# Kernel optimization log

Measured on AMD Instinct MI355X. Metric: run time of the kernel, lower is better.

Reference implementation:

```python
import jax, jax.numpy as jnp
import numpy as np
from jax import lax

BN_EPS = 1e-5


def conv3x3(x, w):
    # x: [B,C,H,W], w: [O,I,3,3] -> [B,O,H,W], stride 1, SAME padding, no bias
    return lax.conv_general_dilated(x, w, (1, 1), 'SAME',
                                    dimension_numbers=('NCHW', 'OIHW', 'NCHW'))


def batchnorm_eval(x, gamma, beta, mean, var):
    inv = gamma / jnp.sqrt(var + BN_EPS)
    return x * inv[None, :, None, None] + (beta - mean * inv)[None, :, None, None]


def avg_pool3(x):
    # AvgPool2d(3, stride=1, padding=1) with count_include_pad=True -> sum/9
    s = lax.reduce_window(x, 0.0, lax.add, (1, 1, 3, 3), (1, 1, 1, 1), 'SAME')
    return s / 9.0


def max_pool3(x):
    return lax.reduce_window(x, -jnp.inf, lax.max, (1, 1, 3, 3), (1, 1, 1, 1), 'SAME')


def setup_inputs() -> dict:
    key = jax.random.key(0)
    ks = jax.random.split(key, 20)
    B, C, H, W = 8, 256, 48, 48
    sc = 0.05
    inp = {
        'ftr': jax.random.normal(ks[0], (B, C, H, W), jnp.float32),
        'wq': jax.random.normal(ks[1], (C, C, 1, 1), jnp.float32) * sc,
        'bq': jax.random.normal(ks[2], (C,), jnp.float32) * sc,
        'wk': jax.random.normal(ks[3], (C, C, 1, 1), jnp.float32) * sc,
        'bk': jax.random.normal(ks[4], (C,), jnp.float32) * sc,
        'wv': jax.random.normal(ks[5], (C, C, 1, 1), jnp.float32) * sc,
        'bv': jax.random.normal(ks[6], (C,), jnp.float32) * sc,
        'delta': jnp.array([0.1], jnp.float32),
        'w_rbc': jax.random.normal(ks[7], (C, C, 3, 3), jnp.float32) * sc,
        'g1': jnp.ones((C,), jnp.float32),
        'b1': jnp.zeros((C,), jnp.float32),
        'm1': jnp.zeros((C,), jnp.float32),
        'v1': jnp.ones((C,), jnp.float32),
        'w_rbc2': jax.random.normal(ks[8], (C, 2 * C, 3, 3), jnp.float32) * sc,
        'g2': jnp.ones((C,), jnp.float32),
        'b2': jnp.zeros((C,), jnp.float32),
        'm2': jnp.zeros((C,), jnp.float32),
        'v2': jnp.ones((C,), jnp.float32),
    }
    return inp


def reference(ftr, wq, bq, wk, bk, wv, bv, delta, w_rbc, g1, b1, m1, v1,
              w_rbc2, g2, b2, m2, v2):
    B, C, H, W = ftr.shape
    P = H * W
    x = ftr.reshape(B, C, P)  # [B,C,P]
    # 1x1 convs as channel matmuls
    q = jnp.einsum('oc,bcp->bop', wq[:, :, 0, 0], x) + bq[None, :, None]
    k = jnp.einsum('oc,bcp->bop', wk[:, :, 0, 0], x) + bk[None, :, None]
    v = jnp.einsum('oc,bcp->bop', wv[:, :, 0, 0], x) + bv[None, :, None]
    # scores[b,i,j] = sum_c q[b,c,i] * k[b,c,j]; softmax over i (dim=1)
    scores = jnp.einsum('bci,bcj->bij', q, k)
    weights = jax.nn.softmax(scores, axis=1)
    G = jnp.einsum('bci,bij->bcj', v, weights).reshape(B, C, H, W)
    out = delta[0] * G + ftr
    # conv_rbc: conv3x3 -> BN(eval) -> ReLU, then sigmoid gate
    out = jax.nn.relu(batchnorm_eval(conv3x3(out, w_rbc), g1, b1, m1, v1))
    gate = jax.nn.sigmoid(out)
    ftr_avg = avg_pool3(ftr) * gate
    ftr_max = max_pool3(ftr) * gate
    cat = jnp.concatenate((ftr_max, ftr_avg), axis=1)  # [B,2C,H,W]
    out = jax.nn.relu(batchnorm_eval(conv3x3(cat, w_rbc2), g2, b2, m2, v2))
    return out
```

## Files before the change

### kernel.cpp

```cpp
#include <hip/hip_runtime.h>
#include <math.h>

#define NB   8
#define CCH  256
#define PPX  2304
#define CPb  (CCH*PPX)
#define NTOT (NB*CPb)
#define PSQ  (PPX*PPX)
#define PADIMG 2500

typedef short short8_t __attribute__((ext_vector_type(8)));
typedef float f4_t __attribute__((ext_vector_type(4)));

__device__ __forceinline__ float relu_(float x){ return x > 0.f ? x : 0.f; }

__device__ __forceinline__ unsigned short f2bf(float f) {
  unsigned int u = __builtin_bit_cast(unsigned int, f);
  u += 0x7fffu + ((u >> 16) & 1u);
  return (unsigned short)(u >> 16);
}
__device__ __forceinline__ float bf2f(unsigned short h) {
  unsigned int u = ((unsigned int)h) << 16;
  return __builtin_bit_cast(float, u);
}
__device__ __forceinline__ unsigned int pack2(float a, float b) {
  return (unsigned int)f2bf(a) | ((unsigned int)f2bf(b) << 16);
}

__device__ __forceinline__ void gll16(const void* g, void* l) {
  __builtin_amdgcn_global_load_lds(
      (const __attribute__((address_space(1))) unsigned int*)g,
      (__attribute__((address_space(3))) unsigned int*)l, 16, 0, 0);
}

__global__ __launch_bounds__(256) void castw(
    const float* __restrict__ w, unsigned short* __restrict__ o, int n)
{
  const int i = blockIdx.x * 256 + threadIdx.x;
  if (i < n) o[i] = f2bf(w[i]);
}

__global__ __launch_bounds__(256) void repack_w(
    const float* __restrict__ w, unsigned short* __restrict__ wr, int Cin)
{
  const int idx = blockIdx.x * 256 + threadIdx.x;
  const int total = 9 * 256 * Cin;
  if (idx >= total) return;
  const int c = idx % Cin;
  const int rest = idx / Cin;
  const int o = rest % 256;
  const int tap = rest / 256;
  wr[idx] = f2bf(w[((size_t)o * Cin + c) * 9 + tap]);
}

__global__ __launch_bounds__(256) void transpose_cast(
    const float* __restrict__ ftr, unsigned short* __restrict__ xt)
{
  const int p0 = blockIdx.x * 64, c0 = blockIdx.y * 64, b = blockIdx.z;
  const int t = threadIdx.x;
  __shared__ unsigned short T[64][72];
  #pragma unroll
  for (int pass = 0; pass < 4; pass++) {
    const int cr = pass * 16 + (t >> 4);
    const int pc = (t & 15) * 4;
    float4 v = *(const float4*)&ftr[((size_t)(b * 256 + c0 + cr)) * PPX + p0 + pc];
    T[pc + 0][cr] = f2bf(v.x); T[pc + 1][cr] = f2bf(v.y);
    T[pc + 2][cr] = f2bf(v.z); T[pc + 3][cr] = f2bf(v.w);
  }
  __syncthreads();
  #pragma unroll
  for (int pass = 0; pass < 2; pass++) {
    const int pr = pass * 32 + (t >> 3);
    const int cc = (t & 7) * 8;
    *(uint4*)&xt[((size_t)(b * PPX + p0 + pr)) * 256 + c0 + cc] = *(const uint4*)&T[pr][cc];
  }
}

template<int EPI>
__global__ __launch_bounds__(256) void gemm_nt(
    const unsigned short* __restrict__ A, long Ab,
    const unsigned short* __restrict__ B, long Bb, int K,
    unsigned short* __restrict__ O, long Ob, int ldo,
    const float* __restrict__ bias,
    const float* __restrict__ ftr, const float* __restrict__ delta, int bstart)
{
  const int t = threadIdx.x;
  const int ln = t & 63;
  const int wid = t >> 6;
  const int wm = (wid & 1) * 64, wn = (wid >> 1) * 64;
  const int lm = ln & 15, lg = ln >> 4;
  const int m0 = blockIdx.x * 128, n0 = blockIdx.y * 128;
  const long bz = blockIdx.z;
  const unsigned short* Ap = A + bz * Ab;
  const unsigned short* Bp = B + bz * Bb;

  __shared__ __align__(16) unsigned short As[128 * 32];
  __shared__ __align__(16) unsigned short Bs[128 * 32];

  const int sR = ln >> 2, sP = ln & 3;
  const int fbase = lm * 32 + (((lg + (lm >> 2)) & 3) * 8);

  f4_t acc[4][4];
  #pragma unroll
  for (int i = 0; i < 4; i++)
    #pragma unroll
    for (int j = 0; j < 4; j++) acc[i][j] = (f4_t){0.f, 0.f, 0.f, 0.f};

  for (int k0 = 0; k0 < K; k0 += 32) {
    __syncthreads();
    #pragma unroll
    for (int i = wid; i < 8; i += 4) {
      const int R = i * 16 + sR;
      const int l = (sP - (R >> 2)) & 3;
      gll16(Ap + (size_t)(m0 + R) * K + k0 + l * 8, As + i * 512);
      gll16(Bp + (size_t)(n0 + R) * K + k0 + l * 8, Bs + i * 512);
    }
    __syncthreads();
    short8_t a[4], b[4];
    #pragma unroll
    for (int ti = 0; ti < 4; ti++)
      a[ti] = *(const short8_t*)(As + (wm + ti * 16) * 32 + fbase);
    #pragma unroll
    for (int tj = 0; tj < 4; tj++)
      b[tj] = *(const short8_t*)(Bs + (wn + tj * 16) * 32 + fbase);
    #pragma unroll
    for (int ti = 0; ti < 4; ti++)
      #pragma unroll
      for (int tj = 0; tj < 4; tj++)
        acc[ti][tj] = __builtin_amdgcn_mfma_f32_16x16x32_bf16(
            a[ti], b[tj], acc[ti][tj], 0, 0, 0);
  }

  if (EPI == 3) {
    const int b = bstart + (int)bz;
    const float d0 = delta[0];
    #pragma unroll
    for (int ti = 0; ti < 4; ti++) {
      const int mb = m0 + wm + ti * 16 + (lg << 2);
      #pragma unroll
      for (int tj = 0; tj < 4; tj++) {
        const int n = n0 + wn + tj * 16 + lm;
        const int y = n / 48, x = n - (n / 48) * 48;
        const size_t pp = (size_t)(y + 1) * 50 + (x + 1);
        float vr[4];
        #pragma unroll
        for (int r = 0; r < 4; r++)
          vr[r] = d0 * acc[ti][tj][r] + ftr[((size_t)(b * 256 + mb + r)) * PPX + n];
        uint2 o;
        o.x = pack2(vr[0], vr[1]);
        o.y = pack2(vr[2], vr[3]);
        *(uint2*)(O + ((size_t)b * PADIMG + pp) * 256 + mb) = o;
      }
    }
  } else {
    #pragma unroll
    for (int ti = 0; ti < 4; ti++) {
      const int mb = m0 + wm + ti * 16 + (lg << 2);
      #pragma unroll
      for (int tj = 0; tj < 4; tj++) {
        const int n = n0 + wn + tj * 16 + lm;
        float add0 = 0.f, add1 = 0.f, add2 = 0.f, add3 = 0.f;
        if (EPI == 1) { add0 = bias[mb]; add1 = bias[mb+1]; add2 = bias[mb+2]; add3 = bias[mb+3]; }
        if (EPI == 2) { add0 = add1 = add2 = add3 = bias[n]; }
        uint2 o;
        o.x = pack2(acc[ti][tj][0] + add0, acc[ti][tj][1] + add1);
        o.y = pack2(acc[ti][tj][2] + add2, acc[ti][tj][3] + add3);
        *(uint2*)(O + bz * Ob + (size_t)n * ldo + mb) = o;
      }
    }
  }
}

__global__ __launch_bounds__(256) void rowstats(
    unsigned short* __restrict__ St, long sstride)
{
  const int j = blockIdx.x, bb = blockIdx.y;
  unsigned short* row = St + (long)bb * sstride + (size_t)j * PPX;
  const int t = threadIdx.x;

  float v[16];
  int nv = 0;
  float m = -1e30f;
  for (int ch = t; ch < 288; ch += 256) {
    const uint4 d = *(const uint4*)(row + ch * 8);
    const unsigned int* dp = (const unsigned int*)&d;
    #pragma unroll
    for (int q = 0; q < 4; q++) {
      v[nv]     = bf2f((unsigned short)(dp[q] & 0xffffu));
      v[nv + 1] = bf2f((unsigned short)(dp[q] >> 16));
      m = fmaxf(m, fmaxf(v[nv], v[nv + 1]));
      nv += 2;
    }
  }
  #pragma unroll
  for (int off = 32; off > 0; off >>= 1)
    m = fmaxf(m, __shfl_xor(m, off));
  __shared__ float red[8];
  if ((t & 63) == 0) red[t >> 6] = m;
  __syncthreads();
  m = fmaxf(fmaxf(red[0], red[1]), fmaxf(red[2], red[3]));

  float sum = 0.f;
  for (int u = 0; u < nv; u++) { v[u] = __expf(v[u] - m); sum += v[u]; }
  #pragma unroll
  for (int off = 32; off > 0; off >>= 1)
    sum += __shfl_xor(sum, off);
  if ((t & 63) == 0) red[4 + (t >> 6)] = sum;
  __syncthreads();
  const float inv = 1.f / (red[4] + red[5] + red[6] + red[7]);

  int u = 0;
  for (int ch = t; ch < 288; ch += 256) {
    unsigned int res[4];
    #pragma unroll
    for (int q = 0; q < 4; q++) {
      res[q] = pack2(v[u] * inv, v[u + 1] * inv);
      u += 2;
    }
    *(uint4*)(row + ch * 8) = *(const uint4*)res;
  }
}

template<bool OUT_BF16>
__global__ __launch_bounds__(128) void conv_mfma(
    const unsigned short* __restrict__ act_p, int Cin,
    const unsigned short* __restrict__ wr,
    const float* __restrict__ gamma, const float* __restrict__ beta,
    const float* __restrict__ mean,  const float* __restrict__ var,
    void* __restrict__ outv)
{
  const int t  = threadIdx.x;
  const int wv = t >> 6;
  const int ln = t & 63;
  const int lm = ln & 15;
  const int lg = ln >> 4;

  const int bx = blockIdx.x;
  const int bb = bx / 18;
  const int p0 = (bx % 18) * 128;
  const int m0 = blockIdx.y * 64;

  __shared__ __align__(16) unsigned short Bs[240 * 32];
  __shared__ __align__(16) unsigned short As[9 * 64 * 32];

  const int qbase = p0 + 2 * (p0 / 48);
  int qoff[4];
  #pragma unroll
  for (int tj = 0; tj < 4; tj++) {
    const int p = p0 + wv * 64 + tj * 16 + lm;
    qoff[tj] = (p - p0) + 2 * (p / 48 - p0 / 48) + 51;
  }

  const int sR = ln >> 2, sP = ln & 3;
  const int abase = lm * 32 + (((lg + (lm >> 2)) & 3) * 8);

  f4_t acc[4][4];
  #pragma unroll
  for (int i = 0; i < 4; i++)
    #pragma unroll
    for (int j = 0; j < 4; j++) acc[i][j] = (f4_t){0.f, 0.f, 0.f, 0.f};

  for (int c0 = 0; c0 < Cin; c0 += 32) {
    __syncthreads();
    const unsigned short* gb = act_p + ((size_t)bb * PADIMG) * Cin + c0;
    for (int i = wv; i < 15; i += 2) {
      const int R = i * 16 + sR;
      int Rg = qbase + R;
      if (Rg > PADIMG - 1) Rg = PADIMG - 1;
      const int l = (sP - (R >> 2)) & 3;
      gll16(gb + (size_t)Rg * Cin + l * 8, Bs + i * 512);
    }
    for (int i = wv; i < 36; i += 2) {
      const int R = i * 16 + sR;
      const int tap = R >> 6, mr = R & 63;
      const int l = (sP - (R >> 2)) & 3;
      gll16(wr + ((size_t)(tap * 256 + m0 + mr)) * Cin + c0 + l * 8, As + i * 512);
    }
    __syncthreads();
    #pragma unroll
    for (int ky = 0; ky < 3; ky++) {
      #pragma unroll
      for (int kx = 0; kx < 3; kx++) {
        const int off = (ky - 1) * 50 + (kx - 1);
        const int tap = ky * 3 + kx;
        short8_t a[4], b[4];
        #pragma unroll
        for (int ti = 0; ti < 4; ti++)
          a[ti] = *(const short8_t*)(As + tap * 2048 + ti * 512 + abase);
        #pragma unroll
        for (int tj = 0; tj < 4; tj++) {
          const int R = qoff[tj] + off;
          const int slot = (lg + (R >> 2)) & 3;
          b[tj] = *(const short8_t*)(Bs + R * 32 + slot * 8);
        }
        #pragma unroll
        for (int ti = 0; ti < 4; ti++)
          #pragma unroll
          for (int tj = 0; tj < 4; tj++)
            acc[ti][tj] = __builtin_amdgcn_mfma_f32_16x16x32_bf16(
                a[ti], b[tj], acc[ti][tj], 0, 0, 0);
      }
    }
  }

  #pragma unroll
  for (int ti = 0; ti < 4; ti++) {
    const int m = m0 + ti * 16 + (lg << 2);
    float inv[4], add[4];
    #pragma unroll
    for (int r = 0; r < 4; r++) {
      inv[r] = gamma[m + r] * rsqrtf(var[m + r] + 1e-5f);
      add[r] = beta[m + r] - mean[m + r] * inv[r];
    }
    #pragma unroll
    for (int tj = 0; tj < 4; tj++) {
      const int p = p0 + wv * 64 + tj * 16 + lm;
      float vr[4];
      #pragma unroll
      for (int r = 0; r < 4; r++)
        vr[r] = relu_(acc[ti][tj][r] * inv[r] + add[r]);
      if (OUT_BF16) {
        uint2 o;
        o.x = pack2(vr[0], vr[1]);
        o.y = pack2(vr[2], vr[3]);
        *(uint2*)((unsigned short*)outv + ((size_t)(bb * PPX + p)) * 256 + m) = o;
      } else {
        #pragma unroll
        for (int r = 0; r < 4; r++)
          ((float*)outv)[((size_t)(bb * 256 + m + r)) * PPX + p] = vr[r];
      }
    }
  }
}

__global__ __launch_bounds__(256) void pool_gate_cat(
    const unsigned short* __restrict__ xt, const unsigned short* __restrict__ act1b,
    unsigned short* __restrict__ cat_p)
{
  const int idx = blockIdx.x * 256 + threadIdx.x;
  const int c = idx & 255;
  const int rest = idx >> 8;
  const int p = rest % PPX;
  const int b = rest / PPX;
  const int y = p / 48, x = p - (p / 48) * 48;
  const unsigned short* base = xt + ((size_t)b * PPX) * 256 + c;
  float s = 0.f, mxv = -1e30f;
  #pragma unroll
  for (int dy = -1; dy <= 1; dy++) {
    const int yy = y + dy;
    if (yy < 0 || yy >= 48) continue;
    #pragma unroll
    for (int dx = -1; dx <= 1; dx++) {
      const int xx = x + dx;
      if (xx < 0 || xx >= 48) continue;
      const float f = bf2f(base[(size_t)(yy * 48 + xx) * 256]);
      s += f; mxv = fmaxf(mxv, f);
    }
  }
  const float g = bf2f(act1b[(size_t)idx]);
  const float gate = 1.f / (1.f + __expf(-g));
  const size_t pp = (size_t)(y + 1) * 50 + (x + 1);
  unsigned short* crow = cat_p + ((size_t)b * PADIMG + pp) * 512;
  crow[c]       = f2bf(mxv * gate);
  crow[c + 256] = f2bf(s * (1.f / 9.f) * gate);
}

extern "C" void kernel_launch(void* const* d_in, const int* in_sizes, int n_in,
                              void* d_out, int out_size, void* d_ws, size_t ws_size,
                              hipStream_t stream)
{
  const float* ftr  = (const float*)d_in[0];
  const float* wq   = (const float*)d_in[1];
  const float* bq   = (const float*)d_in[2];
  const float* wk   = (const float*)d_in[3];
  const float* bk   = (const float*)d_in[4];
  const float* wv   = (const float*)d_in[5];
  const float* bv   = (const float*)d_in[6];
  const float* delta= (const float*)d_in[7];
  const float* w1   = (const float*)d_in[8];
  const float* g1   = (const float*)d_in[9];
  const float* b1   = (const float*)d_in[10];
  const float* m1   = (const float*)d_in[11];
  const float* v1   = (const float*)d_in[12];
  const float* w2   = (const float*)d_in[13];
  const float* g2   = (const float*)d_in[14];
  const float* b2   = (const float*)d_in[15];
  const float* m2   = (const float*)d_in[16];
  const float* v2   = (const float*)d_in[17];
  float* out = (float*)d_out;

  const size_t XT = (size_t)NTOT;
  unsigned short* base = (unsigned short*)d_ws;
  unsigned short* xt   = base;
  unsigned short* qt   = xt  + XT;
  unsigned short* kt   = qt  + XT;
  unsigned short* vbuf = kt  + XT;
  unsigned short* wqb  = vbuf + XT;
  unsigned short* wkb  = wqb + 65536;
  unsigned short* wvb  = wkb + 65536;
  unsigned short* wr1  = wvb + 65536;
  unsigned short* wr2  = wr1 + (size_t)9 * 256 * 256;
  unsigned short* attn_p = wr2 + (size_t)9 * 256 * 512;
  unsigned short* act1b  = attn_p + (size_t)NB * PADIMG * 256;
  unsigned short* cat_p  = act1b + XT;
  unsigned short* St     = cat_p + (size_t)NB * PADIMG * 512;

  const size_t head_bytes = (size_t)((char*)St - (char*)base);
  const bool modeA = ws_size >= head_bytes + (size_t)NB * PSQ * 2;

  const size_t ATTN_P_SH = (size_t)NB * PADIMG * 256;
  const size_t CAT_P_SH  = (size_t)NB * PADIMG * 512;

  castw<<<dim3(256), 256, 0, stream>>>(wq, wqb, 65536);
  castw<<<dim3(256), 256, 0, stream>>>(wk, wkb, 65536);
  castw<<<dim3(256), 256, 0, stream>>>(wv, wvb, 65536);
  repack_w<<<dim3((9 * 256 * 256 + 255) / 256), 256, 0, stream>>>(w1, wr1, 256);
  repack_w<<<dim3((9 * 256 * 512 + 255) / 256), 256, 0, stream>>>(w2, wr2, 512);

  transpose_cast<<<dim3(36, 4, 8), 256, 0, stream>>>(ftr, xt);

  gemm_nt<1><<<dim3(2, 18, 8), 256, 0, stream>>>(
      wqb, 0L, xt, (long)CPb, 256, qt, (long)CPb, 256, bq, nullptr, nullptr, 0);
  gemm_nt<1><<<dim3(2, 18, 8), 256, 0, stream>>>(
      wkb, 0L, xt, (long)CPb, 256, kt, (long)CPb, 256, bk, nullptr, nullptr, 0);
  gemm_nt<2><<<dim3(18, 2, 8), 256, 0, stream>>>(
      xt, (long)CPb, wvb, 0L, 256, vbuf, (long)CPb, PPX, bv, nullptr, nullptr, 0);

  hipMemsetAsync(attn_p, 0, ATTN_P_SH * 2, stream);

  if (modeA) {
    gemm_nt<0><<<dim3(18, 18, 8), 256, 0, stream>>>(
        qt, (long)CPb, kt, (long)CPb, 256, St, (long)PSQ, PPX, nullptr, nullptr, nullptr, 0);
    rowstats<<<dim3(PPX, 8), 256, 0, stream>>>(St, (long)PSQ);
    gemm_nt<3><<<dim3(2, 18, 8), 256, 0, stream>>>(
        vbuf, (long)CPb, St, (long)PSQ, PPX, attn_p, 0L, 0, nullptr, ftr, delta, 0);
  } else {
    for (int b = 0; b < NB; b++) {
      gemm_nt<0><<<dim3(18, 18, 1), 256, 0, stream>>>(
          qt + (size_t)b * CPb, 0L, kt + (size_t)b * CPb, 0L, 256,
          St, 0L, PPX, nullptr, nullptr, nullptr, 0);
      rowstats<<<dim3(PPX, 1), 256, 0, stream>>>(St, 0L);
      gemm_nt<3><<<dim3(2, 18, 1), 256, 0, stream>>>(
          vbuf + (size_t)b * CPb, 0L, St, 0L, PPX, attn_p, 0L, 0, nullptr, ftr, delta, b);
    }
  }

  conv_mfma<true><<<dim3(144, 4), 128, 0, stream>>>(
      attn_p, 256, wr1, g1, b1, m1, v1, (void*)act1b);

  hipMemsetAsync(cat_p, 0, CAT_P_SH * 2, stream);
  pool_gate_cat<<<dim3(NTOT / 256), 256, 0, stream>>>(xt, act1b, cat_p);

  conv_mfma<false><<<dim3(144, 4), 128, 0, stream>>>(
      cat_p, 512, wr2, g2, b2, m2, v2, (void*)out);
}
```

Baseline: 444.0 us.

## Double-buffer conv activation tiles and load weights directly into registers

Restructures the 3x3 conv MFMA kernel to use 256-thread blocks covering 256 pixels by 32 output channels. Weights no longer go through shared memory; each lane loads its A fragments straight from global memory into registers. The activation tile is double-buffered, so the next channel slice's global-to-LDS copy overlaps the current slice's MFMAs, and there is one barrier per iteration instead of two. The cost is heavier register pressure from holding 18 A fragments per lane, plus uncoalesced, redundant global weight reads across blocks.

```diff
diff --git a/kernel.cpp b/kernel.cpp
--- a/kernel.cpp
+++ b/kernel.cpp
@@ -222,7 +222,7 @@
 }
 
 template<bool OUT_BF16>
-__global__ __launch_bounds__(128) void conv_mfma(
+__global__ __launch_bounds__(256, 2) void conv_mfma(
     const unsigned short* __restrict__ act_p, int Cin,
     const unsigned short* __restrict__ wr,
     const float* __restrict__ gamma, const float* __restrict__ beta,
@@ -236,12 +236,11 @@
   const int lg = ln >> 4;
 
   const int bx = blockIdx.x;
-  const int bb = bx / 18;
-  const int p0 = (bx % 18) * 128;
-  const int m0 = blockIdx.y * 64;
-
-  __shared__ __align__(16) unsigned short Bs[240 * 32];
-  __shared__ __align__(16) unsigned short As[9 * 64 * 32];
+  const int bb = bx / 9;
+  const int p0 = (bx % 9) * 256;
+  const int m0 = blockIdx.y * 32;
+
+  __shared__ __align__(16) unsigned short Bs[2][368 * 32];
 
   const int qbase = p0 + 2 * (p0 / 48);
   int qoff[4];
@@ -252,59 +251,65 @@
   }
 
   const int sR = ln >> 2, sP = ln & 3;
-  const int abase = lm * 32 + (((lg + (lm >> 2)) & 3) * 8);
-
-  f4_t acc[4][4];
-  #pragma unroll
-  for (int i = 0; i < 4; i++)
+  const int sl = (sP - (sR >> 2)) & 3;
+
+  const unsigned short* wbase = wr + (size_t)(m0 + lm) * Cin + lg * 8;
+  const unsigned short* gb = act_p + (size_t)bb * PADIMG * Cin;
+  const unsigned short* gsrc = gb + (size_t)(qbase + sR) * Cin + sl * 8;
+
+  f4_t acc[2][4];
+  #pragma unroll
+  for (int i = 0; i < 2; i++)
     #pragma unroll
     for (int j = 0; j < 4; j++) acc[i][j] = (f4_t){0.f, 0.f, 0.f, 0.f};
 
-  for (int c0 = 0; c0 < Cin; c0 += 32) {
-    __syncthreads();
-    const unsigned short* gb = act_p + ((size_t)bb * PADIMG) * Cin + c0;
-    for (int i = wv; i < 15; i += 2) {
-      const int R = i * 16 + sR;
-      int Rg = qbase + R;
-      if (Rg > PADIMG - 1) Rg = PADIMG - 1;
-      const int l = (sP - (R >> 2)) & 3;
-      gll16(gb + (size_t)Rg * Cin + l * 8, Bs + i * 512);
-    }
-    for (int i = wv; i < 36; i += 2) {
-      const int R = i * 16 + sR;
-      const int tap = R >> 6, mr = R & 63;
-      const int l = (sP - (R >> 2)) & 3;
-      gll16(wr + ((size_t)(tap * 256 + m0 + mr)) * Cin + c0 + l * 8, As + i * 512);
-    }
-    __syncthreads();
+  const int nsl = Cin >> 5;
+
+  for (int i = wv; i < 23; i += 4)
+    gll16(gsrc + (size_t)i * 16 * Cin, &Bs[0][i * 512]);
+  __syncthreads();
+
+  int buf = 0;
+  for (int s = 0; s < nsl; s++) {
+    const int c0 = s * 32;
+    short8_t a[9][2];
+    #pragma unroll
+    for (int tap = 0; tap < 9; tap++)
+      #pragma unroll
+      for (int ti = 0; ti < 2; ti++)
+        a[tap][ti] = *(const short8_t*)(wbase + ((size_t)(tap * 256 + ti * 16)) * Cin + c0);
+    if (s + 1 < nsl) {
+      const unsigned short* src = gsrc + (c0 + 32);
+      for (int i = wv; i < 23; i += 4)
+        gll16(src + (size_t)i * 16 * Cin, &Bs[buf ^ 1][i * 512]);
+    }
     #pragma unroll
     for (int ky = 0; ky < 3; ky++) {
       #pragma unroll
       for (int kx = 0; kx < 3; kx++) {
         const int off = (ky - 1) * 50 + (kx - 1);
         const int tap = ky * 3 + kx;
-        short8_t a[4], b[4];
-        #pragma unroll
-        for (int ti = 0; ti < 4; ti++)
-          a[ti] = *(const short8_t*)(As + tap * 2048 + ti * 512 + abase);
+        short8_t b[4];
         #pragma unroll
         for (int tj = 0; tj < 4; tj++) {
           const int R = qoff[tj] + off;
           const int slot = (lg + (R >> 2)) & 3;
-          b[tj] = *(const short8_t*)(Bs + R * 32 + slot * 8);
+          b[tj] = *(const short8_t*)(&Bs[buf][R * 32 + slot * 8]);
         }
         #pragma unroll
-        for (int ti = 0; ti < 4; ti++)
+        for (int ti = 0; ti < 2; ti++)
           #pragma unroll
           for (int tj = 0; tj < 4; tj++)
             acc[ti][tj] = __builtin_amdgcn_mfma_f32_16x16x32_bf16(
-                a[ti], b[tj], acc[ti][tj], 0, 0, 0);
+                a[tap][ti], b[tj], acc[ti][tj], 0, 0, 0);
       }
     }
-  }
-
-  #pragma unroll
-  for (int ti = 0; ti < 4; ti++) {
+    __syncthreads();
+    buf ^= 1;
+  }
+
+  #pragma unroll
+  for (int ti = 0; ti < 2; ti++) {
     const int m = m0 + ti * 16 + (lg << 2);
     float inv[4], add[4];
     #pragma unroll
@@ -445,12 +450,12 @@
     }
   }
 
-  conv_mfma<true><<<dim3(144, 4), 128, 0, stream>>>(
+  conv_mfma<true><<<dim3(72, 8), 256, 0, stream>>>(
       attn_p, 256, wr1, g1, b1, m1, v1, (void*)act1b);
 
   hipMemsetAsync(cat_p, 0, CAT_P_SH * 2, stream);
   pool_gate_cat<<<dim3(NTOT / 256), 256, 0, stream>>>(xt, act1b, cat_p);
 
-  conv_mfma<false><<<dim3(144, 4), 128, 0, stream>>>(
+  conv_mfma<false><<<dim3(72, 8), 256, 0, stream>>>(
       cat_p, 512, wr2, g2, b2, m2, v2, (void*)out);
 }
```

New measurement: 537.7 us. +21.1%, slower.
